# Performance work log

Measured on AMD Instinct MI355X. Metric: run time of the kernel, lower is better.

Reference implementation:

```python
import jax, jax.numpy as jnp
import numpy as np

SEQ = 4096
BLOCK = 64            # sparse_block_size
BLOCKS = SEQ // BLOCK # 64 block rows/cols
NUM_ORACLES = 32
ORACLE = SEQ // NUM_ORACLES      # 128
LOCAL_BLOCKS = ORACLE // BLOCK   # 2 (sliding-window width in blocks)
PATTERN_ID = 0


def _build_block_mask(pattern_id=PATTERN_ID):
    # Mirrors DKernelPredefinedSparseAttention.__init__ create_mask((i,))
    q_pos = np.arange(BLOCKS)[:, None]
    k_pos = np.arange(BLOCKS)[None, :]
    causal = q_pos >= k_pos
    sliding = (q_pos - k_pos) < LOCAL_BLOCKS
    vert = np.zeros(BLOCKS, dtype=bool)
    real_col = int(pattern_id * ORACLE + 0.5)
    cs = real_col // BLOCK
    ce = (real_col + ORACLE) // BLOCK
    vert[cs:ce] = True
    vert[0:1] = True  # global block 0 always visible
    return causal & (sliding | vert[None, :])


def setup_inputs() -> dict:
    key = jax.random.key(0)
    kq, kk, kv = jax.random.split(key, 3)
    shape = (1, SEQ, 8, 128)  # bshd, matches module's own smoke test layout
    q = jax.random.normal(kq, shape, dtype=jnp.float32)
    k = jax.random.normal(kk, shape, dtype=jnp.float32)
    v = jax.random.normal(kv, shape, dtype=jnp.float32)
    block_mask = jnp.asarray(_build_block_mask())  # [BLOCKS, BLOCKS] bool
    return {"q": q, "k": k, "v": v, "block_mask": block_mask}


def reference(q, k, v, block_mask):
    # Expand block-level mask to token level: [S, S]
    tok_mask = jnp.repeat(jnp.repeat(block_mask, BLOCK, axis=0), BLOCK, axis=1)
    scale = 1.0 / jnp.sqrt(jnp.asarray(q.shape[-1], q.dtype))
    # bshd x bshd -> bhqk scores
    scores = jnp.einsum("bqhd,bkhd->bhqk", q, k) * scale
    neg = jnp.asarray(-1e30, scores.dtype)
    scores = jnp.where(tok_mask[None, None, :, :], scores, neg)
    probs = jax.nn.softmax(scores, axis=-1)
    out = jnp.einsum("bhqk,bkhd->bqhd", probs, v)
    return out
```

## Files before the change

kernel.cpp:

```cpp
#include <hip/hip_runtime.h>
#include <hip/hip_bf16.h>

typedef __bf16 bf16x8 __attribute__((ext_vector_type(8)));
typedef float floatx4 __attribute__((ext_vector_type(4)));

constexpr int SEQ = 4096;
constexpr int NH  = 8;
constexpr int DH  = 128;
constexpr int BLK = 64;
constexpr int QBLOCKS = SEQ / BLK;
constexpr int RS = NH * DH;
constexpr float SCALE = 0.088388347648318447f;

__device__ __forceinline__ bf16x8 load8f(const float* p) {
    float4 a = *(const float4*)p;
    float4 b = *(const float4*)(p + 4);
    bf16x8 r = { (__bf16)a.x, (__bf16)a.y, (__bf16)a.z, (__bf16)a.w,
                 (__bf16)b.x, (__bf16)b.y, (__bf16)b.z, (__bf16)b.w };
    return r;
}

__device__ __forceinline__ void stage_v(const float* __restrict__ V,
                                        int kb, int h, int n_t, int kh,
                                        __bf16* __restrict__ dst) {
    const float* base = V + (size_t)(kb * BLK + kh * 32) * RS + h * DH + n_t;
    const int nt = n_t >> 4;
    const int lbase = n_t & 15;
#pragma unroll
    for (int g = 0; g < 4; ++g) {
        bf16x8 pk;
#pragma unroll
        for (int j = 0; j < 8; ++j)
            pk[j] = (__bf16)base[(size_t)(g * 8 + j) * RS];
        __bf16* d = dst + ((size_t)((kh * 8 + nt) * 64 + lbase + 16 * g)) * 8;
        *(bf16x8*)d = pk;
    }
}

__global__ __launch_bounds__(512, 4) void sparse_attn_kernel(
    const float* __restrict__ Q,
    const float* __restrict__ K,
    const float* __restrict__ V,
    float* __restrict__ Out)
{
    const int qb    = blockIdx.x;
    const int h     = blockIdx.y;
    const int tid   = threadIdx.x;
    const int wave  = tid >> 6;
    const int lane  = tid & 63;
    const int strip = wave & 3;
    const int grp   = wave >> 2;
    const int quad  = lane >> 4;
    const int l16   = lane & 15;

    __shared__ __align__(16) __bf16 v_lds[4][2][8][64][8];
    __shared__ __align__(16) __bf16 p_lds[8][16][64];

    int blist[4];
    int nb = 0;
    {
        int cand[4] = {0, 1, qb - 1, qb};
        for (int i = 0; i < 4; ++i) {
            int b = cand[i];
            if (b < 0 || b > qb) continue;
            bool dup = false;
            for (int j = 0; j < nb; ++j) dup = dup || (blist[j] == b);
            if (!dup) blist[nb++] = b;
        }
    }

    {
        const int t256 = tid & 255;
        const int n_t  = t256 & 127;
        const int kh   = t256 >> 7;
        const int half = tid >> 8;
        if (half < nb)
            stage_v(V, blist[half], h, n_t, kh, &v_lds[half][0][0][0][0]);
        if (half + 2 < nb)
            stage_v(V, blist[half + 2], h, n_t, kh, &v_lds[half + 2][0][0][0][0]);
    }

    const int qrow = qb * BLK + strip * 16 + l16;
    const float* qp = Q + (size_t)qrow * RS + h * DH;
    bf16x8 qfrag[4];
#pragma unroll
    for (int s = 0; s < 4; ++s)
        qfrag[s] = load8f(qp + s * 32 + quad * 8);

    floatx4 o_acc[8];
#pragma unroll
    for (int n = 0; n < 8; ++n) o_acc[n] = floatx4{0.f, 0.f, 0.f, 0.f};
    float m_run[4], l_run[4];
#pragma unroll
    for (int r = 0; r < 4; ++r) { m_run[r] = -1e30f; l_run[r] = 0.f; }

    __syncthreads();

#pragma unroll
    for (int it = 0; it < 2; ++it) {
        const int bi = grp + 2 * it;
        if (bi < nb) {
            const int kb = blist[bi];

            floatx4 sfrag[4];
#pragma unroll
            for (int n = 0; n < 4; ++n) {
                floatx4 c = floatx4{0.f, 0.f, 0.f, 0.f};
                const float* kp =
                    K + (size_t)(kb * BLK + n * 16 + l16) * RS + h * DH;
#pragma unroll
                for (int s = 0; s < 4; ++s) {
                    bf16x8 kf = load8f(kp + s * 32 + quad * 8);
                    c = __builtin_amdgcn_mfma_f32_16x16x32_bf16(qfrag[s], kf, c, 0, 0, 0);
                }
                sfrag[n] = c;
            }

            float mnew[4];
#pragma unroll
            for (int r = 0; r < 4; ++r) {
                float mx = m_run[r];
#pragma unroll
                for (int n = 0; n < 4; ++n) {
                    sfrag[n][r] *= SCALE;
                    mx = fmaxf(mx, sfrag[n][r]);
                }
#pragma unroll
                for (int off = 1; off < 16; off <<= 1)
                    mx = fmaxf(mx, __shfl_xor(mx, off, 64));
                mnew[r] = mx;
            }
#pragma unroll
            for (int r = 0; r < 4; ++r) {
                float alpha = __expf(m_run[r] - mnew[r]);
                float rs = 0.f;
#pragma unroll
                for (int n = 0; n < 4; ++n) {
                    float p = __expf(sfrag[n][r] - mnew[r]);
                    sfrag[n][r] = p;
                    rs += p;
                }
#pragma unroll
                for (int off = 1; off < 16; off <<= 1)
                    rs += __shfl_xor(rs, off, 64);
                l_run[r] = l_run[r] * alpha + rs;
                m_run[r] = mnew[r];
#pragma unroll
                for (int n = 0; n < 8; ++n) o_acc[n][r] *= alpha;
            }

#pragma unroll
            for (int n = 0; n < 4; ++n)
#pragma unroll
                for (int r = 0; r < 4; ++r) {
                    const int prow = quad * 4 + r;
                    const int col  = n * 16 + l16;
                    const int idx  = (((col >> 3) ^ (prow & 7)) << 3) | (col & 7);
                    p_lds[wave][prow][idx] = (__bf16)sfrag[n][r];
                }

#pragma unroll
            for (int s2 = 0; s2 < 2; ++s2) {
                bf16x8 pa = *(const bf16x8*)
                    &p_lds[wave][l16][(((s2 * 4 + quad) ^ (l16 & 7)) << 3)];
#pragma unroll
                for (int n = 0; n < 8; ++n) {
                    bf16x8 vb = *(const bf16x8*)&v_lds[bi][s2][n][lane][0];
                    o_acc[n] = __builtin_amdgcn_mfma_f32_16x16x32_bf16(pa, vb, o_acc[n], 0, 0, 0);
                }
            }
        }
    }

    __syncthreads();

    float* mrg = (float*)&v_lds[0][0][0][0][0];
    constexpr int OSTRIDE = 132;
    constexpr int OSZ     = 16 * OSTRIDE;
    constexpr int MBASE   = 4 * OSZ;
    constexpr int LBASE   = MBASE + 64;

    if (grp == 1) {
#pragma unroll
        for (int r = 0; r < 4; ++r) {
            if (l16 == 0) {
                mrg[MBASE + strip * 16 + quad * 4 + r] = m_run[r];
                mrg[LBASE + strip * 16 + quad * 4 + r] = l_run[r];
            }
#pragma unroll
            for (int n = 0; n < 8; ++n)
                mrg[strip * OSZ + (quad * 4 + r) * OSTRIDE + n * 16 + l16] =
                    o_acc[n][r];
        }
    }
    __syncthreads();

    if (grp == 0) {
        const int orow_base = qb * BLK + strip * 16 + quad * 4;
#pragma unroll
        for (int r = 0; r < 4; ++r) {
            const float m1 = mrg[MBASE + strip * 16 + quad * 4 + r];
            const float l1 = mrg[LBASE + strip * 16 + quad * 4 + r];
            const float M  = fmaxf(m_run[r], m1);
            const float a0 = __expf(m_run[r] - M);
            const float a1 = __expf(m1 - M);
            const float inv = 1.f / (a0 * l_run[r] + a1 * l1);
            float* op = Out + (size_t)(orow_base + r) * RS + h * DH + l16;
#pragma unroll
            for (int n = 0; n < 8; ++n) {
                const float o1 =
                    mrg[strip * OSZ + (quad * 4 + r) * OSTRIDE + n * 16 + l16];
                op[n * 16] = (a0 * o_acc[n][r] + a1 * o1) * inv;
            }
        }
    }
}

extern "C" void kernel_launch(void* const* d_in, const int* in_sizes, int n_in,
                              void* d_out, int out_size, void* d_ws, size_t ws_size,
                              hipStream_t stream) {
    const float* Q = (const float*)d_in[0];
    const float* K = (const float*)d_in[1];
    const float* V = (const float*)d_in[2];
    float* Out = (float*)d_out;

    dim3 grid(QBLOCKS, NH);
    dim3 block(512);
    sparse_attn_kernel<<<grid, block, 0, stream>>>(Q, K, V, Out);
}
```

Measured before the change: 127.3 us.

## Split key blocks across four wave groups with a tree merge of partial softmax results

The block grows to 1024 threads so each of up to four groups of four waves handles exactly one visible key block. This replaces the old loop in which two groups each walked two key blocks with an online-softmax rescale. Each group computes its scores, a local max and sum, and its P·V, then partial results are merged pairwise through LDS in two rounds. V staging now runs after the QK MMAs to overlap with them. The goal is to remove the serial per-group iteration, at the cost of extra barriers, a two-stage merge, idle groups on early query blocks, and higher register pressure under the tighter launch bounds.

```diff
diff --git a/kernel.cpp b/kernel.cpp
--- a/kernel.cpp
+++ b/kernel.cpp
@@ -37,7 +37,7 @@
     }
 }
 
-__global__ __launch_bounds__(512, 4) void sparse_attn_kernel(
+__global__ __launch_bounds__(1024, 8) void sparse_attn_kernel(
     const float* __restrict__ Q,
     const float* __restrict__ K,
     const float* __restrict__ V,
@@ -54,7 +54,7 @@
     const int l16   = lane & 15;
 
     __shared__ __align__(16) __bf16 v_lds[4][2][8][64][8];
-    __shared__ __align__(16) __bf16 p_lds[8][16][64];
+    __shared__ __align__(16) __bf16 p_lds[16][16][32];
 
     int blist[4];
     int nb = 0;
@@ -69,147 +69,163 @@
         }
     }
 
-    {
-        const int t256 = tid & 255;
-        const int n_t  = t256 & 127;
-        const int kh   = t256 >> 7;
-        const int half = tid >> 8;
-        if (half < nb)
-            stage_v(V, blist[half], h, n_t, kh, &v_lds[half][0][0][0][0]);
-        if (half + 2 < nb)
-            stage_v(V, blist[half + 2], h, n_t, kh, &v_lds[half + 2][0][0][0][0]);
-    }
-
-    const int qrow = qb * BLK + strip * 16 + l16;
-    const float* qp = Q + (size_t)qrow * RS + h * DH;
-    bf16x8 qfrag[4];
-#pragma unroll
-    for (int s = 0; s < 4; ++s)
-        qfrag[s] = load8f(qp + s * 32 + quad * 8);
+    const bool active = (grp < nb);
+    const int kb = active ? blist[grp] : 0;
 
     floatx4 o_acc[8];
 #pragma unroll
     for (int n = 0; n < 8; ++n) o_acc[n] = floatx4{0.f, 0.f, 0.f, 0.f};
-    float m_run[4], l_run[4];
-#pragma unroll
-    for (int r = 0; r < 4; ++r) { m_run[r] = -1e30f; l_run[r] = 0.f; }
-
-    __syncthreads();
-
-#pragma unroll
-    for (int it = 0; it < 2; ++it) {
-        const int bi = grp + 2 * it;
-        if (bi < nb) {
-            const int kb = blist[bi];
-
-            floatx4 sfrag[4];
+    float m4[4], l4[4];
+#pragma unroll
+    for (int r = 0; r < 4; ++r) { m4[r] = -1e30f; l4[r] = 0.f; }
+
+    floatx4 sfrag[4];
+
+    if (active) {
+        const int qrow = qb * BLK + strip * 16 + l16;
+        const float* qp = Q + (size_t)qrow * RS + h * DH;
+        bf16x8 qfrag[4];
+#pragma unroll
+        for (int s = 0; s < 4; ++s)
+            qfrag[s] = load8f(qp + s * 32 + quad * 8);
+
+#pragma unroll
+        for (int n = 0; n < 4; ++n) {
+            floatx4 c = floatx4{0.f, 0.f, 0.f, 0.f};
+            const float* kp =
+                K + (size_t)(kb * BLK + n * 16 + l16) * RS + h * DH;
+#pragma unroll
+            for (int s = 0; s < 4; ++s) {
+                bf16x8 kf = load8f(kp + s * 32 + quad * 8);
+                c = __builtin_amdgcn_mfma_f32_16x16x32_bf16(qfrag[s], kf, c, 0, 0, 0);
+            }
+            sfrag[n] = c;
+        }
+
+        {
+            const int t256 = tid & 255;
+            stage_v(V, kb, h, t256 & 127, t256 >> 7, &v_lds[grp][0][0][0][0]);
+        }
+
+#pragma unroll
+        for (int r = 0; r < 4; ++r) {
+            float mx = -1e30f;
 #pragma unroll
             for (int n = 0; n < 4; ++n) {
-                floatx4 c = floatx4{0.f, 0.f, 0.f, 0.f};
-                const float* kp =
-                    K + (size_t)(kb * BLK + n * 16 + l16) * RS + h * DH;
-#pragma unroll
-                for (int s = 0; s < 4; ++s) {
-                    bf16x8 kf = load8f(kp + s * 32 + quad * 8);
-                    c = __builtin_amdgcn_mfma_f32_16x16x32_bf16(qfrag[s], kf, c, 0, 0, 0);
-                }
-                sfrag[n] = c;
-            }
-
-            float mnew[4];
-#pragma unroll
-            for (int r = 0; r < 4; ++r) {
-                float mx = m_run[r];
-#pragma unroll
-                for (int n = 0; n < 4; ++n) {
-                    sfrag[n][r] *= SCALE;
-                    mx = fmaxf(mx, sfrag[n][r]);
-                }
-#pragma unroll
-                for (int off = 1; off < 16; off <<= 1)
-                    mx = fmaxf(mx, __shfl_xor(mx, off, 64));
-                mnew[r] = mx;
-            }
-#pragma unroll
-            for (int r = 0; r < 4; ++r) {
-                float alpha = __expf(m_run[r] - mnew[r]);
-                float rs = 0.f;
-#pragma unroll
-                for (int n = 0; n < 4; ++n) {
-                    float p = __expf(sfrag[n][r] - mnew[r]);
-                    sfrag[n][r] = p;
-                    rs += p;
-                }
-#pragma unroll
-                for (int off = 1; off < 16; off <<= 1)
-                    rs += __shfl_xor(rs, off, 64);
-                l_run[r] = l_run[r] * alpha + rs;
-                m_run[r] = mnew[r];
-#pragma unroll
-                for (int n = 0; n < 8; ++n) o_acc[n][r] *= alpha;
-            }
-
-#pragma unroll
-            for (int n = 0; n < 4; ++n)
-#pragma unroll
-                for (int r = 0; r < 4; ++r) {
-                    const int prow = quad * 4 + r;
-                    const int col  = n * 16 + l16;
-                    const int idx  = (((col >> 3) ^ (prow & 7)) << 3) | (col & 7);
-                    p_lds[wave][prow][idx] = (__bf16)sfrag[n][r];
-                }
-
-#pragma unroll
-            for (int s2 = 0; s2 < 2; ++s2) {
-                bf16x8 pa = *(const bf16x8*)
-                    &p_lds[wave][l16][(((s2 * 4 + quad) ^ (l16 & 7)) << 3)];
-#pragma unroll
-                for (int n = 0; n < 8; ++n) {
-                    bf16x8 vb = *(const bf16x8*)&v_lds[bi][s2][n][lane][0];
-                    o_acc[n] = __builtin_amdgcn_mfma_f32_16x16x32_bf16(pa, vb, o_acc[n], 0, 0, 0);
-                }
-            }
-        }
-    }
-
-    __syncthreads();
-
-    float* mrg = (float*)&v_lds[0][0][0][0][0];
-    constexpr int OSTRIDE = 132;
-    constexpr int OSZ     = 16 * OSTRIDE;
-    constexpr int MBASE   = 4 * OSZ;
-    constexpr int LBASE   = MBASE + 64;
-
-    if (grp == 1) {
-#pragma unroll
-        for (int r = 0; r < 4; ++r) {
+                sfrag[n][r] *= SCALE;
+                mx = fmaxf(mx, sfrag[n][r]);
+            }
+#pragma unroll
+            for (int off = 1; off < 16; off <<= 1)
+                mx = fmaxf(mx, __shfl_xor(mx, off, 64));
+            m4[r] = mx;
+        }
+#pragma unroll
+        for (int r = 0; r < 4; ++r) {
+            float rs = 0.f;
+#pragma unroll
+            for (int n = 0; n < 4; ++n) {
+                float p = __expf(sfrag[n][r] - m4[r]);
+                sfrag[n][r] = p;
+                rs += p;
+            }
+#pragma unroll
+            for (int off = 1; off < 16; off <<= 1)
+                rs += __shfl_xor(rs, off, 64);
+            l4[r] = rs;
+        }
+    }
+
+    __syncthreads();
+
+    if (active) {
+#pragma unroll
+        for (int s2 = 0; s2 < 2; ++s2) {
+#pragma unroll
+            for (int nn = 0; nn < 2; ++nn)
+#pragma unroll
+                for (int r = 0; r < 4; ++r)
+                    p_lds[wave][quad * 4 + r][nn * 16 + l16] =
+                        (__bf16)sfrag[s2 * 2 + nn][r];
+            bf16x8 pa = *(const bf16x8*)&p_lds[wave][l16][quad * 8];
+#pragma unroll
+            for (int n = 0; n < 8; ++n) {
+                bf16x8 vb = *(const bf16x8*)&v_lds[grp][s2][n][lane][0];
+                o_acc[n] = __builtin_amdgcn_mfma_f32_16x16x32_bf16(pa, vb, o_acc[n], 0, 0, 0);
+            }
+        }
+    }
+
+    __syncthreads();
+
+    float* scr = (float*)&v_lds[0][0][0][0][0];
+    float* sml = (float*)&p_lds[0][0][0];
+    const int row4 = quad * 4;
+
+    if (grp & 1) {
+        const int reg = grp >> 1;
+        float* ob = scr + reg * 8192 + strip * 2048;
+#pragma unroll
+        for (int r = 0; r < 4; ++r) {
+#pragma unroll
+            for (int n = 0; n < 8; ++n)
+                ob[(row4 + r) * 128 + n * 16 + l16] = o_acc[n][r];
             if (l16 == 0) {
-                mrg[MBASE + strip * 16 + quad * 4 + r] = m_run[r];
-                mrg[LBASE + strip * 16 + quad * 4 + r] = l_run[r];
-            }
+                sml[reg * 128 + strip * 32 + (row4 + r) * 2]     = m4[r];
+                sml[reg * 128 + strip * 32 + (row4 + r) * 2 + 1] = l4[r];
+            }
+        }
+    }
+    __syncthreads();
+
+    if (!(grp & 1)) {
+        const int reg = grp >> 1;
+        const float* ob = scr + reg * 8192 + strip * 2048;
+#pragma unroll
+        for (int r = 0; r < 4; ++r) {
+            const float m1 = sml[reg * 128 + strip * 32 + (row4 + r) * 2];
+            const float l1 = sml[reg * 128 + strip * 32 + (row4 + r) * 2 + 1];
+            const float M  = fmaxf(m4[r], m1);
+            const float a0 = __expf(m4[r] - M);
+            const float a1 = __expf(m1 - M);
+            l4[r] = a0 * l4[r] + a1 * l1;
+            m4[r] = M;
 #pragma unroll
             for (int n = 0; n < 8; ++n)
-                mrg[strip * OSZ + (quad * 4 + r) * OSTRIDE + n * 16 + l16] =
-                    o_acc[n][r];
+                o_acc[n][r] = a0 * o_acc[n][r] +
+                              a1 * ob[(row4 + r) * 128 + n * 16 + l16];
+        }
+    }
+    if (grp == 2) {
+        float* ob = scr + 8192 + strip * 2048;
+#pragma unroll
+        for (int r = 0; r < 4; ++r) {
+#pragma unroll
+            for (int n = 0; n < 8; ++n)
+                ob[(row4 + r) * 128 + n * 16 + l16] = o_acc[n][r];
+            if (l16 == 0) {
+                sml[128 + strip * 32 + (row4 + r) * 2]     = m4[r];
+                sml[128 + strip * 32 + (row4 + r) * 2 + 1] = l4[r];
+            }
         }
     }
     __syncthreads();
 
     if (grp == 0) {
-        const int orow_base = qb * BLK + strip * 16 + quad * 4;
-#pragma unroll
-        for (int r = 0; r < 4; ++r) {
-            const float m1 = mrg[MBASE + strip * 16 + quad * 4 + r];
-            const float l1 = mrg[LBASE + strip * 16 + quad * 4 + r];
-            const float M  = fmaxf(m_run[r], m1);
-            const float a0 = __expf(m_run[r] - M);
+        const float* ob = scr + 8192 + strip * 2048;
+        const int orow_base = qb * BLK + strip * 16 + row4;
+#pragma unroll
+        for (int r = 0; r < 4; ++r) {
+            const float m1 = sml[128 + strip * 32 + (row4 + r) * 2];
+            const float l1 = sml[128 + strip * 32 + (row4 + r) * 2 + 1];
+            const float M  = fmaxf(m4[r], m1);
+            const float a0 = __expf(m4[r] - M);
             const float a1 = __expf(m1 - M);
-            const float inv = 1.f / (a0 * l_run[r] + a1 * l1);
+            const float inv = 1.f / (a0 * l4[r] + a1 * l1);
             float* op = Out + (size_t)(orow_base + r) * RS + h * DH + l16;
 #pragma unroll
             for (int n = 0; n < 8; ++n) {
-                const float o1 =
-                    mrg[strip * OSZ + (quad * 4 + r) * OSTRIDE + n * 16 + l16];
+                const float o1 = ob[(row4 + r) * 128 + n * 16 + l16];
                 op[n * 16] = (a0 * o_acc[n][r] + a1 * o1) * inv;
             }
         }
@@ -225,6 +241,6 @@
     float* Out = (float*)d_out;
 
     dim3 grid(QBLOCKS, NH);
-    dim3 block(512);
+    dim3 block(1024);
     sparse_attn_kernel<<<grid, block, 0, stream>>>(Q, K, V, Out);
 }
```

Result: slower. 154.4 us (+21.3%).

## Compute QK scores for both key blocks before V staging and single-pass softmax

Applied to the files above, without the earlier changes.

Q·K score MFMAs for both of a wave group's key blocks are now issued before V is staged into LDS. This lets the K global loads and matrix work overlap the V staging instead of waiting behind the barrier. The online softmax is replaced by a single max/sum pass over both blocks at once, which removes the alpha rescaling of the output accumulator. The cost is higher register pressure from holding eight score fragments, which may hurt occupancy under the 512x4 launch bound.

```diff
diff --git a/kernel.cpp b/kernel.cpp
--- a/kernel.cpp
+++ b/kernel.cpp
@@ -69,6 +69,43 @@
         }
     }
 
+    const bool v0 = (grp < nb);
+    const bool v1 = (grp + 2 < nb);
+    const int kb0 = v0 ? blist[grp] : 0;
+    const int kb1 = v1 ? blist[grp + 2] : 0;
+
+    const int qrow = qb * BLK + strip * 16 + l16;
+    const float* qp = Q + (size_t)qrow * RS + h * DH;
+    bf16x8 qfrag[4];
+#pragma unroll
+    for (int s = 0; s < 4; ++s)
+        qfrag[s] = load8f(qp + s * 32 + quad * 8);
+
+    floatx4 sfrag[8];
+#pragma unroll
+    for (int t = 0; t < 2; ++t) {
+        const bool valid = t ? v1 : v0;
+        const int  kb    = t ? kb1 : kb0;
+        if (valid) {
+#pragma unroll
+            for (int n = 0; n < 4; ++n) {
+                floatx4 c = floatx4{0.f, 0.f, 0.f, 0.f};
+                const float* kp =
+                    K + (size_t)(kb * BLK + n * 16 + l16) * RS + h * DH;
+#pragma unroll
+                for (int s = 0; s < 4; ++s) {
+                    bf16x8 kf = load8f(kp + s * 32 + quad * 8);
+                    c = __builtin_amdgcn_mfma_f32_16x16x32_bf16(qfrag[s], kf, c, 0, 0, 0);
+                }
+                sfrag[t * 4 + n] = c;
+            }
+        } else {
+#pragma unroll
+            for (int n = 0; n < 4; ++n)
+                sfrag[t * 4 + n] = floatx4{-1e30f, -1e30f, -1e30f, -1e30f};
+        }
+    }
+
     {
         const int t256 = tid & 255;
         const int n_t  = t256 & 127;
@@ -80,94 +117,68 @@
             stage_v(V, blist[half + 2], h, n_t, kh, &v_lds[half + 2][0][0][0][0]);
     }
 
-    const int qrow = qb * BLK + strip * 16 + l16;
-    const float* qp = Q + (size_t)qrow * RS + h * DH;
-    bf16x8 qfrag[4];
-#pragma unroll
-    for (int s = 0; s < 4; ++s)
-        qfrag[s] = load8f(qp + s * 32 + quad * 8);
+    float m4[4], l4[4];
+#pragma unroll
+    for (int r = 0; r < 4; ++r) { m4[r] = -1e30f; l4[r] = 0.f; }
+
+    if (v0) {
+#pragma unroll
+        for (int r = 0; r < 4; ++r) {
+            float mx = -1e30f;
+#pragma unroll
+            for (int i = 0; i < 8; ++i) {
+                sfrag[i][r] *= SCALE;
+                mx = fmaxf(mx, sfrag[i][r]);
+            }
+#pragma unroll
+            for (int off = 1; off < 16; off <<= 1)
+                mx = fmaxf(mx, __shfl_xor(mx, off, 64));
+            m4[r] = mx;
+        }
+#pragma unroll
+        for (int r = 0; r < 4; ++r) {
+            float rs = 0.f;
+#pragma unroll
+            for (int i = 0; i < 8; ++i) {
+                float p = __expf(sfrag[i][r] - m4[r]);
+                sfrag[i][r] = p;
+                rs += p;
+            }
+#pragma unroll
+            for (int off = 1; off < 16; off <<= 1)
+                rs += __shfl_xor(rs, off, 64);
+            l4[r] = rs;
+        }
+    }
 
     floatx4 o_acc[8];
 #pragma unroll
     for (int n = 0; n < 8; ++n) o_acc[n] = floatx4{0.f, 0.f, 0.f, 0.f};
-    float m_run[4], l_run[4];
-#pragma unroll
-    for (int r = 0; r < 4; ++r) { m_run[r] = -1e30f; l_run[r] = 0.f; }
 
     __syncthreads();
 
 #pragma unroll
-    for (int it = 0; it < 2; ++it) {
-        const int bi = grp + 2 * it;
-        if (bi < nb) {
-            const int kb = blist[bi];
-
-            floatx4 sfrag[4];
-#pragma unroll
-            for (int n = 0; n < 4; ++n) {
-                floatx4 c = floatx4{0.f, 0.f, 0.f, 0.f};
-                const float* kp =
-                    K + (size_t)(kb * BLK + n * 16 + l16) * RS + h * DH;
-#pragma unroll
-                for (int s = 0; s < 4; ++s) {
-                    bf16x8 kf = load8f(kp + s * 32 + quad * 8);
-                    c = __builtin_amdgcn_mfma_f32_16x16x32_bf16(qfrag[s], kf, c, 0, 0, 0);
-                }
-                sfrag[n] = c;
-            }
-
-            float mnew[4];
+    for (int t = 0; t < 2; ++t) {
+        const bool valid = t ? v1 : v0;
+        if (!valid) continue;
+        const int bi = grp + 2 * t;
+#pragma unroll
+        for (int n = 0; n < 4; ++n)
 #pragma unroll
             for (int r = 0; r < 4; ++r) {
-                float mx = m_run[r];
-#pragma unroll
-                for (int n = 0; n < 4; ++n) {
-                    sfrag[n][r] *= SCALE;
-                    mx = fmaxf(mx, sfrag[n][r]);
-                }
-#pragma unroll
-                for (int off = 1; off < 16; off <<= 1)
-                    mx = fmaxf(mx, __shfl_xor(mx, off, 64));
-                mnew[r] = mx;
-            }
-#pragma unroll
-            for (int r = 0; r < 4; ++r) {
-                float alpha = __expf(m_run[r] - mnew[r]);
-                float rs = 0.f;
-#pragma unroll
-                for (int n = 0; n < 4; ++n) {
-                    float p = __expf(sfrag[n][r] - mnew[r]);
-                    sfrag[n][r] = p;
-                    rs += p;
-                }
-#pragma unroll
-                for (int off = 1; off < 16; off <<= 1)
-                    rs += __shfl_xor(rs, off, 64);
-                l_run[r] = l_run[r] * alpha + rs;
-                m_run[r] = mnew[r];
-#pragma unroll
-                for (int n = 0; n < 8; ++n) o_acc[n][r] *= alpha;
-            }
-
-#pragma unroll
-            for (int n = 0; n < 4; ++n)
-#pragma unroll
-                for (int r = 0; r < 4; ++r) {
-                    const int prow = quad * 4 + r;
-                    const int col  = n * 16 + l16;
-                    const int idx  = (((col >> 3) ^ (prow & 7)) << 3) | (col & 7);
-                    p_lds[wave][prow][idx] = (__bf16)sfrag[n][r];
-                }
-
-#pragma unroll
-            for (int s2 = 0; s2 < 2; ++s2) {
-                bf16x8 pa = *(const bf16x8*)
-                    &p_lds[wave][l16][(((s2 * 4 + quad) ^ (l16 & 7)) << 3)];
-#pragma unroll
-                for (int n = 0; n < 8; ++n) {
-                    bf16x8 vb = *(const bf16x8*)&v_lds[bi][s2][n][lane][0];
-                    o_acc[n] = __builtin_amdgcn_mfma_f32_16x16x32_bf16(pa, vb, o_acc[n], 0, 0, 0);
-                }
+                const int prow = quad * 4 + r;
+                const int col  = n * 16 + l16;
+                const int idx  = (((col >> 3) ^ (prow & 7)) << 3) | (col & 7);
+                p_lds[wave][prow][idx] = (__bf16)sfrag[t * 4 + n][r];
+            }
+#pragma unroll
+        for (int s2 = 0; s2 < 2; ++s2) {
+            bf16x8 pa = *(const bf16x8*)
+                &p_lds[wave][l16][(((s2 * 4 + quad) ^ (l16 & 7)) << 3)];
+#pragma unroll
+            for (int n = 0; n < 8; ++n) {
+                bf16x8 vb = *(const bf16x8*)&v_lds[bi][s2][n][lane][0];
+                o_acc[n] = __builtin_amdgcn_mfma_f32_16x16x32_bf16(pa, vb, o_acc[n], 0, 0, 0);
             }
         }
     }
@@ -184,8 +195,8 @@
 #pragma unroll
         for (int r = 0; r < 4; ++r) {
             if (l16 == 0) {
-                mrg[MBASE + strip * 16 + quad * 4 + r] = m_run[r];
-                mrg[LBASE + strip * 16 + quad * 4 + r] = l_run[r];
+                mrg[MBASE + strip * 16 + quad * 4 + r] = m4[r];
+                mrg[LBASE + strip * 16 + quad * 4 + r] = l4[r];
             }
 #pragma unroll
             for (int n = 0; n < 8; ++n)
@@ -201,10 +212,10 @@
         for (int r = 0; r < 4; ++r) {
             const float m1 = mrg[MBASE + strip * 16 + quad * 4 + r];
             const float l1 = mrg[LBASE + strip * 16 + quad * 4 + r];
-            const float M  = fmaxf(m_run[r], m1);
-            const float a0 = __expf(m_run[r] - M);
+            const float M  = fmaxf(m4[r], m1);
+            const float a0 = __expf(m4[r] - M);
             const float a1 = __expf(m1 - M);
-            const float inv = 1.f / (a0 * l_run[r] + a1 * l1);
+            const float inv = 1.f / (a0 * l4[r] + a1 * l1);
             float* op = Out + (size_t)(orow_base + r) * RS + h * DH + l16;
 #pragma unroll
             for (int n = 0; n < 8; ++n) {
```

Result: no change. 126.4 us (-0.7%).

## Split work per 16-row strip, one wave per key block, drop V staging

Applied to the files above, without the earlier changes.

Grid grows fourfold so each workgroup handles a single 16-row query strip, with one wave per visible key block (up to 4) instead of 8 waves that looped over blocks. V is now read straight from global memory into MFMA B fragments, so the shared-memory V staging pass and its barrier go away. Partial outputs are merged in LDS with a single log-sum-exp combine across up to four waves. The costs are reloading K and V once per strip (four times more global reads for those blocks) and strided, uncoalesced per-element V loads.

```diff
diff --git a/kernel.cpp b/kernel.cpp
--- a/kernel.cpp
+++ b/kernel.cpp
@@ -20,41 +20,24 @@
     return r;
 }
 
-__device__ __forceinline__ void stage_v(const float* __restrict__ V,
-                                        int kb, int h, int n_t, int kh,
-                                        __bf16* __restrict__ dst) {
-    const float* base = V + (size_t)(kb * BLK + kh * 32) * RS + h * DH + n_t;
-    const int nt = n_t >> 4;
-    const int lbase = n_t & 15;
-#pragma unroll
-    for (int g = 0; g < 4; ++g) {
-        bf16x8 pk;
-#pragma unroll
-        for (int j = 0; j < 8; ++j)
-            pk[j] = (__bf16)base[(size_t)(g * 8 + j) * RS];
-        __bf16* d = dst + ((size_t)((kh * 8 + nt) * 64 + lbase + 16 * g)) * 8;
-        *(bf16x8*)d = pk;
-    }
-}
-
-__global__ __launch_bounds__(512, 4) void sparse_attn_kernel(
+__global__ __launch_bounds__(256, 4) void sparse_attn_kernel(
     const float* __restrict__ Q,
     const float* __restrict__ K,
     const float* __restrict__ V,
     float* __restrict__ Out)
 {
-    const int qb    = blockIdx.x;
+    const int qb    = blockIdx.x >> 2;
+    const int strip = blockIdx.x & 3;
     const int h     = blockIdx.y;
     const int tid   = threadIdx.x;
     const int wave  = tid >> 6;
     const int lane  = tid & 63;
-    const int strip = wave & 3;
-    const int grp   = wave >> 2;
     const int quad  = lane >> 4;
     const int l16   = lane & 15;
 
-    __shared__ __align__(16) __bf16 v_lds[4][2][8][64][8];
-    __shared__ __align__(16) __bf16 p_lds[8][16][64];
+    __shared__ __align__(16) __bf16 p_lds[4][16][64];
+    __shared__ float mrg[3][16][130];
+    __shared__ float ml[3][16][2];
 
     int blist[4];
     int nb = 0;
@@ -69,149 +52,144 @@
         }
     }
 
-    {
-        const int t256 = tid & 255;
-        const int n_t  = t256 & 127;
-        const int kh   = t256 >> 7;
-        const int half = tid >> 8;
-        if (half < nb)
-            stage_v(V, blist[half], h, n_t, kh, &v_lds[half][0][0][0][0]);
-        if (half + 2 < nb)
-            stage_v(V, blist[half + 2], h, n_t, kh, &v_lds[half + 2][0][0][0][0]);
+    const bool active = (wave < nb);
+    const int kb = active ? blist[wave] : 0;
+
+    float m4[4], l4[4];
+    floatx4 o_acc[8];
+#pragma unroll
+    for (int n = 0; n < 8; ++n) o_acc[n] = floatx4{0.f, 0.f, 0.f, 0.f};
+#pragma unroll
+    for (int r = 0; r < 4; ++r) { m4[r] = -1e30f; l4[r] = 0.f; }
+
+    if (active) {
+        const int qrow = qb * BLK + strip * 16 + l16;
+        const float* qp = Q + (size_t)qrow * RS + h * DH;
+        bf16x8 qfrag[4];
+#pragma unroll
+        for (int s = 0; s < 4; ++s)
+            qfrag[s] = load8f(qp + s * 32 + quad * 8);
+
+        floatx4 sfrag[4];
+#pragma unroll
+        for (int n = 0; n < 4; ++n) {
+            floatx4 c = floatx4{0.f, 0.f, 0.f, 0.f};
+            const float* kp =
+                K + (size_t)(kb * BLK + n * 16 + l16) * RS + h * DH;
+#pragma unroll
+            for (int s = 0; s < 4; ++s) {
+                bf16x8 kf = load8f(kp + s * 32 + quad * 8);
+                c = __builtin_amdgcn_mfma_f32_16x16x32_bf16(qfrag[s], kf, c, 0, 0, 0);
+            }
+            sfrag[n] = c;
+        }
+
+#pragma unroll
+        for (int r = 0; r < 4; ++r) {
+            float mx = -1e30f;
+#pragma unroll
+            for (int n = 0; n < 4; ++n) {
+                sfrag[n][r] *= SCALE;
+                mx = fmaxf(mx, sfrag[n][r]);
+            }
+#pragma unroll
+            for (int off = 1; off < 16; off <<= 1)
+                mx = fmaxf(mx, __shfl_xor(mx, off, 64));
+            m4[r] = mx;
+        }
+#pragma unroll
+        for (int r = 0; r < 4; ++r) {
+            float rs = 0.f;
+#pragma unroll
+            for (int n = 0; n < 4; ++n) {
+                float p = __expf(sfrag[n][r] - m4[r]);
+                sfrag[n][r] = p;
+                rs += p;
+            }
+#pragma unroll
+            for (int off = 1; off < 16; off <<= 1)
+                rs += __shfl_xor(rs, off, 64);
+            l4[r] = rs;
+        }
+
+#pragma unroll
+        for (int n = 0; n < 4; ++n)
+#pragma unroll
+            for (int r = 0; r < 4; ++r) {
+                const int prow = quad * 4 + r;
+                const int col  = n * 16 + l16;
+                const int idx  = (((col >> 3) ^ (prow & 7)) << 3) | (col & 7);
+                p_lds[wave][prow][idx] = (__bf16)sfrag[n][r];
+            }
+
+        const float* vp = V + (size_t)(kb * BLK) * RS + h * DH;
+#pragma unroll
+        for (int s2 = 0; s2 < 2; ++s2) {
+            bf16x8 pa = *(const bf16x8*)
+                &p_lds[wave][l16][(((s2 * 4 + quad) ^ (l16 & 7)) << 3)];
+#pragma unroll
+            for (int n = 0; n < 8; ++n) {
+                const float* vpp =
+                    vp + (size_t)(s2 * 32 + quad * 8) * RS + n * 16 + l16;
+                float tv[8];
+#pragma unroll
+                for (int j = 0; j < 8; ++j)
+                    tv[j] = vpp[(size_t)j * RS];
+                bf16x8 vb = { (__bf16)tv[0], (__bf16)tv[1], (__bf16)tv[2],
+                              (__bf16)tv[3], (__bf16)tv[4], (__bf16)tv[5],
+                              (__bf16)tv[6], (__bf16)tv[7] };
+                o_acc[n] = __builtin_amdgcn_mfma_f32_16x16x32_bf16(pa, vb, o_acc[n], 0, 0, 0);
+            }
+        }
+
+        if (wave > 0) {
+            float* ob = &mrg[wave - 1][0][0];
+#pragma unroll
+            for (int r = 0; r < 4; ++r) {
+                const int row = quad * 4 + r;
+#pragma unroll
+                for (int n = 0; n < 8; ++n)
+                    ob[row * 130 + n * 16 + l16] = o_acc[n][r];
+                if (l16 == 0) {
+                    ml[wave - 1][row][0] = m4[r];
+                    ml[wave - 1][row][1] = l4[r];
+                }
+            }
+        }
     }
 
-    const int qrow = qb * BLK + strip * 16 + l16;
-    const float* qp = Q + (size_t)qrow * RS + h * DH;
-    bf16x8 qfrag[4];
-#pragma unroll
-    for (int s = 0; s < 4; ++s)
-        qfrag[s] = load8f(qp + s * 32 + quad * 8);
-
-    floatx4 o_acc[8];
-#pragma unroll
-    for (int n = 0; n < 8; ++n) o_acc[n] = floatx4{0.f, 0.f, 0.f, 0.f};
-    float m_run[4], l_run[4];
-#pragma unroll
-    for (int r = 0; r < 4; ++r) { m_run[r] = -1e30f; l_run[r] = 0.f; }
-
     __syncthreads();
 
-#pragma unroll
-    for (int it = 0; it < 2; ++it) {
-        const int bi = grp + 2 * it;
-        if (bi < nb) {
-            const int kb = blist[bi];
-
-            floatx4 sfrag[4];
-#pragma unroll
-            for (int n = 0; n < 4; ++n) {
-                floatx4 c = floatx4{0.f, 0.f, 0.f, 0.f};
-                const float* kp =
-                    K + (size_t)(kb * BLK + n * 16 + l16) * RS + h * DH;
-#pragma unroll
-                for (int s = 0; s < 4; ++s) {
-                    bf16x8 kf = load8f(kp + s * 32 + quad * 8);
-                    c = __builtin_amdgcn_mfma_f32_16x16x32_bf16(qfrag[s], kf, c, 0, 0, 0);
+    if (wave == 0) {
+        const int orow_base = qb * BLK + strip * 16 + quad * 4;
+#pragma unroll
+        for (int r = 0; r < 4; ++r) {
+            const int row = quad * 4 + r;
+            float M = m4[r];
+#pragma unroll
+            for (int j = 1; j < 4; ++j)
+                if (j < nb) M = fmaxf(M, ml[j - 1][row][0]);
+            const float a0 = __expf(m4[r] - M);
+            float lsum = a0 * l4[r];
+            float o[8];
+#pragma unroll
+            for (int n = 0; n < 8; ++n) o[n] = a0 * o_acc[n][r];
+#pragma unroll
+            for (int j = 1; j < 4; ++j) {
+                if (j < nb) {
+                    const float aj = __expf(ml[j - 1][row][0] - M);
+                    lsum += aj * ml[j - 1][row][1];
+                    const float* ob = &mrg[j - 1][0][0];
+#pragma unroll
+                    for (int n = 0; n < 8; ++n)
+                        o[n] += aj * ob[row * 130 + n * 16 + l16];
                 }
-                sfrag[n] = c;
-            }
-
-            float mnew[4];
-#pragma unroll
-            for (int r = 0; r < 4; ++r) {
-                float mx = m_run[r];
-#pragma unroll
-                for (int n = 0; n < 4; ++n) {
-                    sfrag[n][r] *= SCALE;
-                    mx = fmaxf(mx, sfrag[n][r]);
-                }
-#pragma unroll
-                for (int off = 1; off < 16; off <<= 1)
-                    mx = fmaxf(mx, __shfl_xor(mx, off, 64));
-                mnew[r] = mx;
-            }
-#pragma unroll
-            for (int r = 0; r < 4; ++r) {
-                float alpha = __expf(m_run[r] - mnew[r]);
-                float rs = 0.f;
-#pragma unroll
-                for (int n = 0; n < 4; ++n) {
-                    float p = __expf(sfrag[n][r] - mnew[r]);
-                    sfrag[n][r] = p;
-                    rs += p;
-                }
-#pragma unroll
-                for (int off = 1; off < 16; off <<= 1)
-                    rs += __shfl_xor(rs, off, 64);
-                l_run[r] = l_run[r] * alpha + rs;
-                m_run[r] = mnew[r];
-#pragma unroll
-                for (int n = 0; n < 8; ++n) o_acc[n][r] *= alpha;
-            }
-
-#pragma unroll
-            for (int n = 0; n < 4; ++n)
-#pragma unroll
-                for (int r = 0; r < 4; ++r) {
-                    const int prow = quad * 4 + r;
-                    const int col  = n * 16 + l16;
-                    const int idx  = (((col >> 3) ^ (prow & 7)) << 3) | (col & 7);
-                    p_lds[wave][prow][idx] = (__bf16)sfrag[n][r];
-                }
-
-#pragma unroll
-            for (int s2 = 0; s2 < 2; ++s2) {
-                bf16x8 pa = *(const bf16x8*)
-                    &p_lds[wave][l16][(((s2 * 4 + quad) ^ (l16 & 7)) << 3)];
-#pragma unroll
-                for (int n = 0; n < 8; ++n) {
-                    bf16x8 vb = *(const bf16x8*)&v_lds[bi][s2][n][lane][0];
-                    o_acc[n] = __builtin_amdgcn_mfma_f32_16x16x32_bf16(pa, vb, o_acc[n], 0, 0, 0);
-                }
-            }
-        }
-    }
-
-    __syncthreads();
-
-    float* mrg = (float*)&v_lds[0][0][0][0][0];
-    constexpr int OSTRIDE = 132;
-    constexpr int OSZ     = 16 * OSTRIDE;
-    constexpr int MBASE   = 4 * OSZ;
-    constexpr int LBASE   = MBASE + 64;
-
-    if (grp == 1) {
-#pragma unroll
-        for (int r = 0; r < 4; ++r) {
-            if (l16 == 0) {
-                mrg[MBASE + strip * 16 + quad * 4 + r] = m_run[r];
-                mrg[LBASE + strip * 16 + quad * 4 + r] = l_run[r];
-            }
+            }
+            const float inv = 1.f / lsum;
+            float* op = Out + (size_t)(orow_base + r) * RS + h * DH + l16;
 #pragma unroll
             for (int n = 0; n < 8; ++n)
-                mrg[strip * OSZ + (quad * 4 + r) * OSTRIDE + n * 16 + l16] =
-                    o_acc[n][r];
-        }
-    }
-    __syncthreads();
-
-    if (grp == 0) {
-        const int orow_base = qb * BLK + strip * 16 + quad * 4;
-#pragma unroll
-        for (int r = 0; r < 4; ++r) {
-            const float m1 = mrg[MBASE + strip * 16 + quad * 4 + r];
-            const float l1 = mrg[LBASE + strip * 16 + quad * 4 + r];
-            const float M  = fmaxf(m_run[r], m1);
-            const float a0 = __expf(m_run[r] - M);
-            const float a1 = __expf(m1 - M);
-            const float inv = 1.f / (a0 * l_run[r] + a1 * l1);
-            float* op = Out + (size_t)(orow_base + r) * RS + h * DH + l16;
-#pragma unroll
-            for (int n = 0; n < 8; ++n) {
-                const float o1 =
-                    mrg[strip * OSZ + (quad * 4 + r) * OSTRIDE + n * 16 + l16];
-                op[n * 16] = (a0 * o_acc[n][r] + a1 * o1) * inv;
-            }
+                op[n * 16] = o[n] * inv;
         }
     }
 }
@@ -224,7 +202,7 @@
     const float* V = (const float*)d_in[2];
     float* Out = (float*)d_out;
 
-    dim3 grid(QBLOCKS, NH);
-    dim3 block(512);
+    dim3 grid(QBLOCKS * 4, NH);
+    dim3 block(256);
     sparse_attn_kernel<<<grid, block, 0, stream>>>(Q, K, V, Out);
 }
```

After: 157.6 us. +23.8%, slower.
